# Kernel tuning notes

Measured on AMD Instinct MI355X. Metric: run time of the kernel, lower is better.

## Reference

```python
import jax, jax.numpy as jnp
import numpy as np

N = 50000        # total nodes (disjoint batch of graphs)
E = 800000       # total edges
F_IN = 8         # node feature dim
S = 6            # edge feature dim
H = 20           # ECC kernel-network hidden size (hidden_states)
N_OUT = 20       # ECC output channels (n_out=hidden_states)
G = 32           # GCN channels
D1 = 16          # first dense
N_GRAPHS = 512   # graphs in batch


def setup_inputs() -> dict:
    key = jax.random.key(0)
    ks = jax.random.split(key, 24)
    r = lambda k, sh, s: jax.random.normal(k, sh, dtype=jnp.float32) * s
    return {
        "x": r(ks[0], (N, F_IN), 1.0),
        "e": r(ks[1], (E, S), 1.0),
        "edge_index": jax.random.randint(ks[2], (2, E), 0, N, dtype=jnp.int32),
        "seg": jnp.sort(jax.random.randint(ks[3], (N,), 0, N_GRAPHS, dtype=jnp.int32)),
        # ECC kernel network: S -> H -> H -> F_IN*N_OUT
        "ecc_w1": r(ks[4], (S, H), 0.4), "ecc_b1": jnp.zeros((H,), jnp.float32),
        "ecc_w2": r(ks[5], (H, H), 0.2), "ecc_b2": jnp.zeros((H,), jnp.float32),
        "ecc_w3": r(ks[6], (H, F_IN * N_OUT), 0.2), "ecc_b3": jnp.zeros((F_IN * N_OUT,), jnp.float32),
        "ecc_root": r(ks[7], (F_IN, N_OUT), 0.3), "ecc_b": jnp.zeros((N_OUT,), jnp.float32),
        "gcn1_w": r(ks[8], (N_OUT, G), 0.2), "gcn1_b": jnp.zeros((G,), jnp.float32),
        "gcn2_w": r(ks[9], (G, G), 0.2), "gcn2_b": jnp.zeros((G,), jnp.float32),
        "d1_w": r(ks[10], (G, D1), 0.2), "d1_b": jnp.zeros((D1,), jnp.float32),
        "d2_w": r(ks[11], (D1, 1), 0.2), "d2_b": jnp.zeros((1,), jnp.float32),
    }


def reference(x, e, edge_index, seg,
              ecc_w1, ecc_b1, ecc_w2, ecc_b2, ecc_w3, ecc_b3, ecc_root, ecc_b,
              gcn1_w, gcn1_b, gcn2_w, gcn2_b, d1_w, d1_b, d2_w, d2_b):
    row, col = edge_index[0], edge_index[1]  # message col -> row

    # --- ECCConv: per-edge MLP produces an [F_IN, N_OUT] filter per edge ---
    h = jax.nn.relu(e @ ecc_w1 + ecc_b1)
    h = jax.nn.relu(h @ ecc_w2 + ecc_b2)
    w_edge = (h @ ecc_w3 + ecc_b3).reshape(E, F_IN, N_OUT)   # [E, F_in, F_out]
    msg = jnp.einsum('ef,efo->eo', x[col], w_edge)            # per-edge message
    agg = jax.ops.segment_sum(msg, row, num_segments=N)
    x1 = jax.nn.relu(agg + x @ ecc_root + ecc_b)              # root + bias + relu

    # --- GCN normalization from the edge list (A + I, symmetric norm) ---
    deg = jax.ops.segment_sum(jnp.ones((E,), x.dtype), row, num_segments=N) + 1.0
    dinv = jax.lax.rsqrt(deg)
    edge_norm = (dinv[row] * dinv[col])[:, None]
    self_norm = (dinv * dinv)[:, None]

    def gcn(hin, W, b):
        hw = hin @ W
        nmsg = jax.ops.segment_sum(edge_norm * hw[col], row, num_segments=N)
        return jax.nn.relu(nmsg + self_norm * hw + b)

    x2 = gcn(x1, gcn1_w, gcn1_b)
    x3 = gcn(x2, gcn2_w, gcn2_b)

    # --- GlobalSumPool over graph ids, then MLP head ---
    pooled = jax.ops.segment_sum(x3, seg, num_segments=N_GRAPHS)  # [n_graphs, G]
    out = (pooled @ d1_w + d1_b) @ d2_w + d2_b                    # [n_graphs, 1]
    return out
```

## Files before the change

kernel.cpp:

```cpp
#include <hip/hip_runtime.h>

#define S_DIM   6
#define H_DIM   20
#define F_INN   8
#define N_OUTC  20
#define G_DIM   32
#define D1_DIM  16
#define NGRAPH  512
#define CAP     32
#define COLCAP  2048

typedef short short8 __attribute__((ext_vector_type(8)));
typedef float floatx4 __attribute__((ext_vector_type(4)));

__device__ __forceinline__ unsigned short f2bf(float f) {
    unsigned u = __float_as_uint(f);
    return (unsigned short)((u + 0x8000u) >> 16);
}
__device__ __forceinline__ float bf2f(unsigned short s) {
    return __uint_as_float(((unsigned)s) << 16);
}

__global__ __launch_bounds__(256) void loc_kernel(
    const int* __restrict__ ei, int E, int* __restrict__ cnt,
    int* __restrict__ loc,
    const float* __restrict__ w3, const float* __restrict__ b3,
    unsigned short* __restrict__ B3f)
{
    int i = blockIdx.x * 256 + threadIdx.x;
    if (i < 6144) {
        int jj   = i & 7;
        int n    = (i >> 3) & 15;
        int quad = (i >> 7) & 3;
        int nt   = (i >> 9) & 1;
        int s    = i >> 10;
        int K = 32 * s + quad * 8 + jj;
        int o = n + 16 * nt;
        float v = 0.0f;
        if (o < N_OUTC) {
            if (K < 160)      v = w3[(K >> 3) * 160 + (K & 7) * N_OUTC + o];
            else if (K < 168) v = b3[(K - 160) * N_OUTC + o];
        }
        B3f[i] = f2bf(v);
    }
    if (i >= E) return;
    loc[i] = atomicAdd(&cnt[ei[i]], 1);
}

__global__ __launch_bounds__(256) void scanA_kernel(
    const int* __restrict__ deg, int N, int* __restrict__ bsum)
{
    int i = blockIdx.x * 256 + threadIdx.x;
    int v = (i < N) ? deg[i] : 0;
#pragma unroll
    for (int d = 1; d < 64; d <<= 1) v += __shfl_down(v, d, 64);
    __shared__ int ws[4];
    int wid = threadIdx.x >> 6;
    if ((threadIdx.x & 63) == 0) ws[wid] = v;
    __syncthreads();
    if (threadIdx.x == 0) bsum[blockIdx.x] = ws[0] + ws[1] + ws[2] + ws[3];
}

__global__ __launch_bounds__(256) void scanC_kernel(
    const int* __restrict__ deg, int N, const int* __restrict__ bsum, int nbl,
    int E, int* __restrict__ rowptr)
{
    __shared__ int ws[4];
    __shared__ int sboff;
    int t = threadIdx.x;
    {
        int v = (t < nbl && t < blockIdx.x) ? bsum[t] : 0;
#pragma unroll
        for (int d = 1; d < 64; d <<= 1) v += __shfl_down(v, d, 64);
        int wid = t >> 6;
        if ((t & 63) == 0) ws[wid] = v;
        __syncthreads();
        if (t == 0) sboff = ws[0] + ws[1] + ws[2] + ws[3];
        __syncthreads();
    }

    int i = blockIdx.x * 256 + t;
    int d0 = (i < N) ? deg[i] : 0;
    int v = d0;
#pragma unroll
    for (int d = 1; d < 64; d <<= 1) {
        int u = __shfl_up(v, d, 64);
        if ((t & 63) >= d) v += u;
    }
    __shared__ int ws2[4];
    int wid = t >> 6;
    if ((t & 63) == 63) ws2[wid] = v;
    __syncthreads();
    int woff = 0;
    for (int w = 0; w < wid; ++w) woff += ws2[w];
    if (i < N) rowptr[i] = sboff + woff + v - d0;
    if (blockIdx.x == 0 && t == 0) rowptr[N] = E;
}

__global__ __launch_bounds__(256) void build_kernel(
    const int* __restrict__ ei, int E, const float* __restrict__ e,
    const int* __restrict__ rowptr, const int* __restrict__ loc,
    int4* __restrict__ e_sorted)
{
    int i = blockIdx.x * 256 + threadIdx.x;
    if (i >= E) return;
    int r = ei[i];
    int c = ei[E + i];
    int p = rowptr[r] + loc[i];

    const float2* ep = (const float2*)&e[(size_t)i * S_DIM];
    float2 e0 = ep[0], e1 = ep[1], e2 = ep[2];

    int4 rec;
    rec.x = c;
    rec.y = (int)f2bf(e0.x) | ((int)f2bf(e0.y) << 16);
    rec.z = (int)f2bf(e1.x) | ((int)f2bf(e1.y) << 16);
    rec.w = (int)f2bf(e2.x) | ((int)f2bf(e2.y) << 16);
    e_sorted[p] = rec;
}

__global__ __launch_bounds__(256) void ecc_mfma_kernel(
    const int4* __restrict__ e_sorted, const float* __restrict__ x,
    const int* __restrict__ rowptr, int N, int E,
    const unsigned short* __restrict__ B3f,
    const float* __restrict__ w1, const float* __restrict__ b1,
    const float* __restrict__ w2, const float* __restrict__ b2,
    const float* __restrict__ root, const float* __restrict__ eb,
    const float* __restrict__ g1w,
    float* __restrict__ agg, int* __restrict__ col_sorted,
    unsigned short* __restrict__ hws1)
{
    __shared__ char smem[20480];
    __shared__ float x1buf[CAP * N_OUTC];
    __shared__ int rbounds[2];
    unsigned short (*h2b)[N_OUTC] = (unsigned short (*)[N_OUTC])smem;
    unsigned short (*xb)[F_INN]   = (unsigned short (*)[F_INN])(smem + 10240);
    float* lmsg = (float*)smem;

    int t = threadIdx.x;
    int j0 = blockIdx.x * 256;
    int jend = min(j0 + 256, E);
    int j = j0 + t;

    if (t < 2) {
        int s = (t == 0) ? j0 : (jend - 1);
        int lo = 0, hi = N - 1;
        while (lo < hi) {
            int m = (lo + hi + 1) >> 1;
            if (rowptr[m] <= s) lo = m; else hi = m - 1;
        }
        rbounds[t] = lo;
    }

    if (j < E) {
        int4 rec = e_sorted[j];
        int c = rec.x;
        col_sorted[j] = c;
        float ef[S_DIM] = {
            bf2f((unsigned short)(rec.y & 0xffff)),
            bf2f((unsigned short)((unsigned)rec.y >> 16)),
            bf2f((unsigned short)(rec.z & 0xffff)),
            bf2f((unsigned short)((unsigned)rec.z >> 16)),
            bf2f((unsigned short)(rec.w & 0xffff)),
            bf2f((unsigned short)((unsigned)rec.w >> 16))
        };

        float h1[H_DIM];
#pragma unroll
        for (int jj = 0; jj < H_DIM; ++jj) {
            float a = b1[jj];
#pragma unroll
            for (int s = 0; s < S_DIM; ++s) a = fmaf(ef[s], w1[s * H_DIM + jj], a);
            h1[jj] = fmaxf(a, 0.0f);
        }

        float h2[H_DIM];
#pragma unroll
        for (int jj = 0; jj < H_DIM; ++jj) {
            float a = b2[jj];
#pragma unroll
            for (int k = 0; k < H_DIM; ++k) a = fmaf(h1[k], w2[k * H_DIM + jj], a);
            h2[jj] = fmaxf(a, 0.0f);
        }

        const float4* xp = (const float4*)&x[(size_t)c * F_INN];
        float4 xa = xp[0], xb4 = xp[1];
        float xf[F_INN] = {xa.x, xa.y, xa.z, xa.w, xb4.x, xb4.y, xb4.z, xb4.w};

#pragma unroll
        for (int o = 0; o < N_OUTC; ++o) h2b[t][o] = f2bf(h2[o]);
#pragma unroll
        for (int f = 0; f < F_INN; ++f) xb[t][f] = f2bf(xf[f]);
    } else {
#pragma unroll
        for (int o = 0; o < N_OUTC; ++o) h2b[t][o] = 0;
#pragma unroll
        for (int f = 0; f < F_INN; ++f) xb[t][f] = 0;
    }
    __syncthreads();

    int lane = t & 63;
    int quad = lane >> 4;
    int n = lane & 15;
    const short8* Bg = (const short8*)B3f;
    short8 Bf[12];
#pragma unroll
    for (int s = 0; s < 6; ++s)
#pragma unroll
        for (int nt = 0; nt < 2; ++nt)
            Bf[s * 2 + nt] = Bg[((s * 2 + nt) * 4 + quad) * 16 + n];

    int w = t >> 6;
    floatx4 acc0s[4], acc1s[4];
#pragma unroll
    for (int T = 0; T < 4; ++T) {
        int base = w * 64 + T * 16;
        int m = base + n;

        const short8 xv8 = *(const short8*)&xb[m][0];
        float xfl[F_INN];
#pragma unroll
        for (int jj = 0; jj < F_INN; ++jj) xfl[jj] = bf2f((unsigned short)xv8[jj]);

        floatx4 acc0 = {0.f, 0.f, 0.f, 0.f};
        floatx4 acc1 = {0.f, 0.f, 0.f, 0.f};
#pragma unroll
        for (int s = 0; s < 6; ++s) {
            short8 A = {0, 0, 0, 0, 0, 0, 0, 0};
            if (s < 5) {
                float h = bf2f(h2b[m][4 * s + quad]);
#pragma unroll
                for (int jj = 0; jj < F_INN; ++jj)
                    A[jj] = (short)f2bf(h * xfl[jj]);
            } else if (quad == 0) {
                A = xv8;
            }
            acc0 = __builtin_amdgcn_mfma_f32_16x16x32_bf16(A, Bf[s * 2 + 0], acc0, 0, 0, 0);
            acc1 = __builtin_amdgcn_mfma_f32_16x16x32_bf16(A, Bf[s * 2 + 1], acc1, 0, 0, 0);
        }
        acc0s[T] = acc0;
        acc1s[T] = acc1;
    }
    __syncthreads();

#pragma unroll
    for (int T = 0; T < 4; ++T) {
        int base = w * 64 + T * 16;
#pragma unroll
        for (int r = 0; r < 4; ++r) {
            int row = base + quad * 4 + r;
            lmsg[row * N_OUTC + n] = acc0s[T][r];
            if (n < 4) lmsg[row * N_OUTC + 16 + n] = acc1s[T][r];
        }
    }
    __syncthreads();

    int r0 = rbounds[0], r1 = rbounds[1];
    int nrows = r1 - r0 + 1;
    int work = nrows * 5;
    for (int ww = t; ww < work; ww += 256) {
        int idx = ww / 5;
        int q = ww - idx * 5;
        int row = r0 + idx;
        int a0 = rowptr[row], a1 = rowptr[row + 1];
        int s0 = max(a0, j0), s1 = min(a1, jend);
        float ac0 = 0.f, ac1 = 0.f, ac2 = 0.f, ac3 = 0.f;
        for (int s = s0; s < s1; ++s) {
            const float4 v = *(const float4*)&lmsg[(s - j0) * N_OUTC + q * 4];
            ac0 += v.x; ac1 += v.y; ac2 += v.z; ac3 += v.w;
        }
        bool owned = (a0 >= j0 && a1 <= jend);
        if (owned && idx < CAP) {
            const float4* xp = (const float4*)&x[(size_t)row * F_INN];
            float4 xa = xp[0], xb4 = xp[1];
            float rx[F_INN] = {xa.x, xa.y, xa.z, xa.w, xb4.x, xb4.y, xb4.z, xb4.w};
            float av[4] = {ac0, ac1, ac2, ac3};
#pragma unroll
            for (int u = 0; u < 4; ++u) {
                int oc = q * 4 + u;
                float a = av[u] + eb[oc];
#pragma unroll
                for (int f = 0; f < F_INN; ++f)
                    a = fmaf(rx[f], root[f * N_OUTC + oc], a);
                x1buf[idx * N_OUTC + oc] = fmaxf(a, 0.0f);
            }
        } else {
            float* dst = &agg[(size_t)row * N_OUTC + q * 4];
            if (owned) {
                *(float4*)dst = make_float4(ac0, ac1, ac2, ac3);
            } else {
                unsafeAtomicAdd(dst + 0, ac0);
                unsafeAtomicAdd(dst + 1, ac1);
                unsafeAtomicAdd(dst + 2, ac2);
                unsafeAtomicAdd(dst + 3, ac3);
            }
        }
    }
    __syncthreads();

    int fast = min(nrows, CAP);
    int work2 = fast * 8;
    for (int ww = t; ww < work2; ww += 256) {
        int idx = ww >> 3;
        int qc = ww & 7;
        int row = r0 + idx;
        int a0 = rowptr[row], a1 = rowptr[row + 1];
        if (!(a0 >= j0 && a1 <= jend)) continue;
        float di = rsqrtf((float)(a1 - a0) + 1.0f);
        float m0 = 0.f, m1 = 0.f, m2 = 0.f, m3 = 0.f;
        const float* xr = &x1buf[idx * N_OUTC];
#pragma unroll
        for (int o = 0; o < N_OUTC; ++o) {
            float xv = xr[o];
            const float4 g = *(const float4*)&g1w[o * G_DIM + qc * 4];
            m0 = fmaf(xv, g.x, m0); m1 = fmaf(xv, g.y, m1);
            m2 = fmaf(xv, g.z, m2); m3 = fmaf(xv, g.w, m3);
        }
        unsigned lo32 = (unsigned)f2bf(m0 * di) | ((unsigned)f2bf(m1 * di) << 16);
        unsigned hi32 = (unsigned)f2bf(m2 * di) | ((unsigned)f2bf(m3 * di) << 16);
        *(uint2*)&hws1[(size_t)row * G_DIM + qc * 4] = make_uint2(lo32, hi32);
    }
}

__global__ __launch_bounds__(256) void cleanup_kernel(
    const float* __restrict__ agg, const float* __restrict__ x,
    const int* __restrict__ rowptr, int N,
    const float* __restrict__ root, const float* __restrict__ eb,
    const float* __restrict__ g1w,
    unsigned short* __restrict__ hws1)
{
    int n = blockIdx.x * 256 + threadIdx.x;
    if (n >= N) return;
    int a0 = rowptr[n], a1 = rowptr[n + 1];
    bool contained = (a1 > a0) ? ((a0 >> 8) == ((a1 - 1) >> 8))
                               : ((a0 & 255) != 0);
    if (contained) {
        int target = (a0 >> 8) << 8;
        int lo = 0, hi = N - 1;
        while (lo < hi) {
            int m = (lo + hi + 1) >> 1;
            if (rowptr[m] <= target) lo = m; else hi = m - 1;
        }
        if (n - lo < CAP) return;
    }

    const float4* xp = (const float4*)&x[(size_t)n * F_INN];
    float4 xa = xp[0], xb = xp[1];
    float xf[F_INN] = {xa.x, xa.y, xa.z, xa.w, xb.x, xb.y, xb.z, xb.w};

    float x1[N_OUTC];
#pragma unroll
    for (int o = 0; o < N_OUTC; ++o) {
        float a = agg[(size_t)n * N_OUTC + o] + eb[o];
#pragma unroll
        for (int f = 0; f < F_INN; ++f) a = fmaf(xf[f], root[f * N_OUTC + o], a);
        x1[o] = fmaxf(a, 0.0f);
    }

    float di = rsqrtf((float)(a1 - a0) + 1.0f);
#pragma unroll
    for (int q = 0; q < 4; ++q) {
        short8 o8;
#pragma unroll
        for (int u = 0; u < 8; ++u) {
            int g = q * 8 + u;
            float a = 0.0f;
#pragma unroll
            for (int o = 0; o < N_OUTC; ++o) a = fmaf(x1[o], g1w[o * G_DIM + g], a);
            o8[u] = (short)f2bf(a * di);
        }
        *(short8*)&hws1[(size_t)n * G_DIM + q * 8] = o8;
    }
}

template<bool DO_MATMUL, bool DO_POOL>
__global__ __launch_bounds__(256) void gcn_gather_kernel(
    const unsigned short* __restrict__ hws, const int* __restrict__ rowptr,
    const int* __restrict__ col_sorted, const int* __restrict__ seg, int N,
    const float* __restrict__ bias, const float* __restrict__ w2,
    unsigned short* __restrict__ outbuf, float* __restrict__ pooled)
{
    __shared__ int colbuf[COLCAP];
    __shared__ int binfo[2];
    __shared__ float x2s[DO_MATMUL ? 64 * 33 : 1];
    __shared__ float w2s[DO_MATMUL ? G_DIM * G_DIM : 1];
    __shared__ float pbuf[DO_POOL ? 64 * G_DIM : 1];
    __shared__ int ginfo[2];

    int t = threadIdx.x;
    int n0 = blockIdx.x * 64;
    int nend = min(n0 + 64, N);

    if (t == 0) { binfo[0] = rowptr[n0]; binfo[1] = rowptr[nend]; }
    if (DO_MATMUL) ((float4*)w2s)[t] = ((const float4*)w2)[t];
    if (DO_POOL) {
        if (t == 0) {
            int gmin = seg[n0];
            int gmax = seg[nend - 1];
            ginfo[0] = gmin;
            ginfo[1] = (gmax - gmin < 64) ? 1 : 0;
        }
        for (int k = t; k < 64 * G_DIM; k += 256) pbuf[k] = 0.0f;
    }
    __syncthreads();

    int jb0 = binfo[0];
    int cap = min(binfo[1] - jb0, COLCAP);
    for (int k = t; k < cap; k += 256) colbuf[k] = col_sorted[jb0 + k];
    __syncthreads();

    int nl = t >> 2;
    int q = t & 3;
    int n = n0 + nl;

    float xo[8];
    float di = 0.0f;
    if (n < N) {
        int j0 = rowptr[n], j1 = rowptr[n + 1];
        di = rsqrtf((float)(j1 - j0) + 1.0f);
        short8 sv = *(const short8*)&hws[(size_t)n * G_DIM + q * 8];
        float s[8];
#pragma unroll
        for (int k = 0; k < 8; ++k) s[k] = bf2f((unsigned short)sv[k]);
#pragma unroll 2
        for (int j = j0; j < j1; ++j) {
            int idx = j - jb0;
            int c = (idx < COLCAP) ? colbuf[idx] : col_sorted[j];
            short8 v = *(const short8*)&hws[(size_t)c * G_DIM + q * 8];
#pragma unroll
            for (int k = 0; k < 8; ++k) s[k] += bf2f((unsigned short)v[k]);
        }
#pragma unroll
        for (int k = 0; k < 8; ++k)
            xo[k] = fmaxf(fmaf(di, s[k], bias[q * 8 + k]), 0.0f);
    } else {
#pragma unroll
        for (int k = 0; k < 8; ++k) xo[k] = 0.0f;
    }

    if (DO_MATMUL) {
#pragma unroll
        for (int k = 0; k < 8; ++k) x2s[nl * 33 + q * 8 + k] = xo[k];
        __syncthreads();
        if (n < N) {
            float a[8];
#pragma unroll
            for (int k = 0; k < 8; ++k) a[k] = 0.0f;
#pragma unroll
            for (int g = 0; g < G_DIM; ++g) {
                float xv = x2s[nl * 33 + g];
#pragma unroll
                for (int k = 0; k < 8; ++k)
                    a[k] = fmaf(xv, w2s[g * G_DIM + q * 8 + k], a[k]);
            }
            short8 o8;
#pragma unroll
            for (int k = 0; k < 8; ++k) o8[k] = (short)f2bf(a[k] * di);
            *(short8*)&outbuf[(size_t)n * G_DIM + q * 8] = o8;
        }
    } else if (DO_POOL) {
        int gmin = ginfo[0];
        int use_lds = ginfo[1];
        if (n < N) {
            int sg = seg[n];
            if (use_lds) {
                float* base = &pbuf[(sg - gmin) * G_DIM + q * 8];
#pragma unroll
                for (int k = 0; k < 8; ++k) atomicAdd(&base[k], xo[k]);
            } else {
#pragma unroll
                for (int k = 0; k < 8; ++k)
                    unsafeAtomicAdd(&pooled[(size_t)sg * G_DIM + q * 8 + k], xo[k]);
            }
        }
        __syncthreads();
        if (use_lds) {
            for (int k = t; k < 64 * G_DIM; k += 256) {
                float v = pbuf[k];
                int g = gmin + (k >> 5);
                if (v != 0.0f && g < NGRAPH)
                    unsafeAtomicAdd(&pooled[(size_t)g * G_DIM + (k & 31)], v);
            }
        }
    } else {
        if (n < N) {
            short8 o8;
#pragma unroll
            for (int k = 0; k < 8; ++k) o8[k] = (short)f2bf(xo[k]);
            *(short8*)&outbuf[(size_t)n * G_DIM + q * 8] = o8;
        }
    }
}

__global__ __launch_bounds__(256) void head_kernel(
    const float* __restrict__ pooled,
    const float* __restrict__ d1w, const float* __restrict__ d1b,
    const float* __restrict__ d2w, const float* __restrict__ d2b,
    float* __restrict__ out)
{
    int i = blockIdx.x * 256 + threadIdx.x;
    if (i >= NGRAPH) return;

    float p[G_DIM];
#pragma unroll
    for (int g = 0; g < G_DIM; ++g) p[g] = pooled[i * G_DIM + g];

    float acc = d2b[0];
#pragma unroll
    for (int j = 0; j < D1_DIM; ++j) {
        float tj = d1b[j];
#pragma unroll
        for (int g = 0; g < G_DIM; ++g) tj = fmaf(p[g], d1w[g * D1_DIM + j], tj);
        acc = fmaf(tj, d2w[j], acc);
    }
    out[i] = acc;
}

extern "C" void kernel_launch(void* const* d_in, const int* in_sizes, int n_in,
                              void* d_out, int out_size, void* d_ws, size_t ws_size,
                              hipStream_t stream)
{
    const float* x    = (const float*)d_in[0];
    const float* e    = (const float*)d_in[1];
    const int*   ei   = (const int*)d_in[2];
    const int*   seg  = (const int*)d_in[3];
    const float* w1   = (const float*)d_in[4];
    const float* b1   = (const float*)d_in[5];
    const float* w2   = (const float*)d_in[6];
    const float* b2   = (const float*)d_in[7];
    const float* w3   = (const float*)d_in[8];
    const float* b3   = (const float*)d_in[9];
    const float* root = (const float*)d_in[10];
    const float* eb   = (const float*)d_in[11];
    const float* g1w  = (const float*)d_in[12];
    const float* g1b  = (const float*)d_in[13];
    const float* g2w  = (const float*)d_in[14];
    const float* g2b  = (const float*)d_in[15];
    const float* d1w  = (const float*)d_in[16];
    const float* d1b  = (const float*)d_in[17];
    const float* d2w  = (const float*)d_in[18];
    const float* d2b  = (const float*)d_in[19];

    const int N = in_sizes[3];
    const int E = in_sizes[1] / S_DIM;
    float* out = (float*)d_out;

    const int nbl = (N + 255) / 256;
    const int ebl = (E + 255) / 256;

    char* ws = (char*)d_ws;
    size_t off = 0;
    auto alloc = [&](size_t elems) -> char* {
        char* p = ws + off;
        off += ((elems * 4 + 15) & ~(size_t)15);
        return p;
    };
    int*   cnt        = (int*)  alloc(N);
    float* agg        = (float*)alloc((size_t)N * N_OUTC);
    float* pooled     = (float*)alloc(NGRAPH * G_DIM);
    size_t zero_bytes = off;
    int*   rowptr     = (int*)  alloc(N + 1);
    int*   bsum       = (int*)  alloc(nbl);
    int*   loc        = (int*)  alloc(E);
    int*   col_sorted = (int*)  alloc(E);
    unsigned short* B3f = (unsigned short*)alloc(6144 / 2);
    int4*  e_sorted   = (int4*) alloc((size_t)E * 4);
    unsigned short* hws1 = (unsigned short*)alloc((size_t)N * G_DIM / 2);
    unsigned short* hws2 = (unsigned short*)alloc((size_t)N * G_DIM / 2);
    (void)ws_size;

    hipMemsetAsync(d_ws, 0, zero_bytes, stream);

    loc_kernel<<<ebl, 256, 0, stream>>>(ei, E, cnt, loc, w3, b3, B3f);
    scanA_kernel<<<nbl, 256, 0, stream>>>(cnt, N, bsum);
    scanC_kernel<<<nbl, 256, 0, stream>>>(cnt, N, bsum, nbl, E, rowptr);
    build_kernel<<<ebl, 256, 0, stream>>>(ei, E, e, rowptr, loc, e_sorted);
    ecc_mfma_kernel<<<ebl, 256, 0, stream>>>(e_sorted, x, rowptr, N, E, B3f,
                                             w1, b1, w2, b2, root, eb, g1w,
                                             agg, col_sorted, hws1);
    cleanup_kernel<<<nbl, 256, 0, stream>>>(agg, x, rowptr, N, root, eb, g1w, hws1);
    gcn_gather_kernel<true, false><<<(N + 63) / 64, 256, 0, stream>>>(
        hws1, rowptr, col_sorted, seg, N, g1b, g2w, hws2, nullptr);
    gcn_gather_kernel<false, true><<<(N + 63) / 64, 256, 0, stream>>>(
        hws2, rowptr, col_sorted, seg, N, g2b, nullptr, nullptr, pooled);
    head_kernel<<<(NGRAPH + 255) / 256, 256, 0, stream>>>(pooled, d1w, d1b, d2w, d2b, out);
}
```

Before: 267.1 us.

## Use cursor atomics for CSR build, packed bf16 converts, unrolled GCN gather

The per-edge loc array is dropped. The histogram kernel now only counts, and the build kernel claims CSR slots with an atomic cursor initialised during the scan, which saves one E-sized write and read. All float-to-bf16 conversions switch to the packed round-to-nearest intrinsic. The GCN gather drops its LDS column staging and reads col_sorted directly, unrolled by four to expose more independent loads. The cursor atomics make the order of edges within a row nondeterministic, and the extra atomic traffic in the build kernel could cost about as much as it saves.

```diff
diff --git a/kernel.cpp b/kernel.cpp
--- a/kernel.cpp
+++ b/kernel.cpp
@@ -1,4 +1,5 @@
 #include <hip/hip_runtime.h>
+#include <hip/hip_bf16.h>
 
 #define S_DIM   6
 #define H_DIM   20
@@ -8,7 +9,6 @@
 #define D1_DIM  16
 #define NGRAPH  512
 #define CAP     32
-#define COLCAP  2048
 
 typedef short short8 __attribute__((ext_vector_type(8)));
 typedef float floatx4 __attribute__((ext_vector_type(4)));
@@ -20,10 +20,14 @@
 __device__ __forceinline__ float bf2f(unsigned short s) {
     return __uint_as_float(((unsigned)s) << 16);
 }
-
-__global__ __launch_bounds__(256) void loc_kernel(
+__device__ __forceinline__ unsigned pk2bf(float a, float b) {
+    union { __hip_bfloat162 b2; unsigned u; } cv;
+    cv.b2 = __float22bfloat162_rn(make_float2(a, b));
+    return cv.u;
+}
+
+__global__ __launch_bounds__(256) void hist_kernel(
     const int* __restrict__ ei, int E, int* __restrict__ cnt,
-    int* __restrict__ loc,
     const float* __restrict__ w3, const float* __restrict__ b3,
     unsigned short* __restrict__ B3f)
 {
@@ -44,7 +48,7 @@
         B3f[i] = f2bf(v);
     }
     if (i >= E) return;
-    loc[i] = atomicAdd(&cnt[ei[i]], 1);
+    atomicAdd(&cnt[ei[i]], 1);
 }
 
 __global__ __launch_bounds__(256) void scanA_kernel(
@@ -63,7 +67,7 @@
 
 __global__ __launch_bounds__(256) void scanC_kernel(
     const int* __restrict__ deg, int N, const int* __restrict__ bsum, int nbl,
-    int E, int* __restrict__ rowptr)
+    int E, int* __restrict__ rowptr, int* __restrict__ cursor)
 {
     __shared__ int ws[4];
     __shared__ int sboff;
@@ -93,29 +97,32 @@
     __syncthreads();
     int woff = 0;
     for (int w = 0; w < wid; ++w) woff += ws2[w];
-    if (i < N) rowptr[i] = sboff + woff + v - d0;
+    if (i < N) {
+        int rp = sboff + woff + v - d0;
+        rowptr[i] = rp;
+        cursor[i] = rp;
+    }
     if (blockIdx.x == 0 && t == 0) rowptr[N] = E;
 }
 
 __global__ __launch_bounds__(256) void build_kernel(
     const int* __restrict__ ei, int E, const float* __restrict__ e,
-    const int* __restrict__ rowptr, const int* __restrict__ loc,
-    int4* __restrict__ e_sorted)
+    int* __restrict__ cursor, int4* __restrict__ e_sorted)
 {
     int i = blockIdx.x * 256 + threadIdx.x;
     if (i >= E) return;
     int r = ei[i];
     int c = ei[E + i];
-    int p = rowptr[r] + loc[i];
+    int p = atomicAdd(&cursor[r], 1);
 
     const float2* ep = (const float2*)&e[(size_t)i * S_DIM];
     float2 e0 = ep[0], e1 = ep[1], e2 = ep[2];
 
     int4 rec;
     rec.x = c;
-    rec.y = (int)f2bf(e0.x) | ((int)f2bf(e0.y) << 16);
-    rec.z = (int)f2bf(e1.x) | ((int)f2bf(e1.y) << 16);
-    rec.w = (int)f2bf(e2.x) | ((int)f2bf(e2.y) << 16);
+    rec.y = (int)pk2bf(e0.x, e0.y);
+    rec.z = (int)pk2bf(e1.x, e1.y);
+    rec.w = (int)pk2bf(e2.x, e2.y);
     e_sorted[p] = rec;
 }
 
@@ -188,14 +195,16 @@
         float xf[F_INN] = {xa.x, xa.y, xa.z, xa.w, xb4.x, xb4.y, xb4.z, xb4.w};
 
 #pragma unroll
-        for (int o = 0; o < N_OUTC; ++o) h2b[t][o] = f2bf(h2[o]);
-#pragma unroll
-        for (int f = 0; f < F_INN; ++f) xb[t][f] = f2bf(xf[f]);
+        for (int p = 0; p < N_OUTC / 2; ++p)
+            *(unsigned*)&h2b[t][2 * p] = pk2bf(h2[2 * p], h2[2 * p + 1]);
+#pragma unroll
+        for (int p = 0; p < F_INN / 2; ++p)
+            *(unsigned*)&xb[t][2 * p] = pk2bf(xf[2 * p], xf[2 * p + 1]);
     } else {
 #pragma unroll
-        for (int o = 0; o < N_OUTC; ++o) h2b[t][o] = 0;
-#pragma unroll
-        for (int f = 0; f < F_INN; ++f) xb[t][f] = 0;
+        for (int p = 0; p < N_OUTC / 2; ++p) *(unsigned*)&h2b[t][2 * p] = 0u;
+#pragma unroll
+        for (int p = 0; p < F_INN / 2; ++p)  *(unsigned*)&xb[t][2 * p] = 0u;
     }
     __syncthreads();
 
@@ -229,9 +238,11 @@
             short8 A = {0, 0, 0, 0, 0, 0, 0, 0};
             if (s < 5) {
                 float h = bf2f(h2b[m][4 * s + quad]);
-#pragma unroll
-                for (int jj = 0; jj < F_INN; ++jj)
-                    A[jj] = (short)f2bf(h * xfl[jj]);
+                union { short8 s8; unsigned u[4]; } av;
+#pragma unroll
+                for (int p = 0; p < 4; ++p)
+                    av.u[p] = pk2bf(h * xfl[2 * p], h * xfl[2 * p + 1]);
+                A = av.s8;
             } else if (quad == 0) {
                 A = xv8;
             }
@@ -316,8 +327,8 @@
             m0 = fmaf(xv, g.x, m0); m1 = fmaf(xv, g.y, m1);
             m2 = fmaf(xv, g.z, m2); m3 = fmaf(xv, g.w, m3);
         }
-        unsigned lo32 = (unsigned)f2bf(m0 * di) | ((unsigned)f2bf(m1 * di) << 16);
-        unsigned hi32 = (unsigned)f2bf(m2 * di) | ((unsigned)f2bf(m3 * di) << 16);
+        unsigned lo32 = pk2bf(m0 * di, m1 * di);
+        unsigned hi32 = pk2bf(m2 * di, m3 * di);
         *(uint2*)&hws1[(size_t)row * G_DIM + qc * 4] = make_uint2(lo32, hi32);
     }
 }
@@ -360,16 +371,19 @@
     float di = rsqrtf((float)(a1 - a0) + 1.0f);
 #pragma unroll
     for (int q = 0; q < 4; ++q) {
-        short8 o8;
+        float a[8];
 #pragma unroll
         for (int u = 0; u < 8; ++u) {
             int g = q * 8 + u;
-            float a = 0.0f;
-#pragma unroll
-            for (int o = 0; o < N_OUTC; ++o) a = fmaf(x1[o], g1w[o * G_DIM + g], a);
-            o8[u] = (short)f2bf(a * di);
-        }
-        *(short8*)&hws1[(size_t)n * G_DIM + q * 8] = o8;
+            float acc = 0.0f;
+#pragma unroll
+            for (int o = 0; o < N_OUTC; ++o) acc = fmaf(x1[o], g1w[o * G_DIM + g], acc);
+            a[u] = acc * di;
+        }
+        union { short8 s8; unsigned u4[4]; } ov;
+#pragma unroll
+        for (int p = 0; p < 4; ++p) ov.u4[p] = pk2bf(a[2 * p], a[2 * p + 1]);
+        *(short8*)&hws1[(size_t)n * G_DIM + q * 8] = ov.s8;
     }
 }
 
@@ -380,8 +394,6 @@
     const float* __restrict__ bias, const float* __restrict__ w2,
     unsigned short* __restrict__ outbuf, float* __restrict__ pooled)
 {
-    __shared__ int colbuf[COLCAP];
-    __shared__ int binfo[2];
     __shared__ float x2s[DO_MATMUL ? 64 * 33 : 1];
     __shared__ float w2s[DO_MATMUL ? G_DIM * G_DIM : 1];
     __shared__ float pbuf[DO_POOL ? 64 * G_DIM : 1];
@@ -391,7 +403,6 @@
     int n0 = blockIdx.x * 64;
     int nend = min(n0 + 64, N);
 
-    if (t == 0) { binfo[0] = rowptr[n0]; binfo[1] = rowptr[nend]; }
     if (DO_MATMUL) ((float4*)w2s)[t] = ((const float4*)w2)[t];
     if (DO_POOL) {
         if (t == 0) {
@@ -402,12 +413,7 @@
         }
         for (int k = t; k < 64 * G_DIM; k += 256) pbuf[k] = 0.0f;
     }
-    __syncthreads();
-
-    int jb0 = binfo[0];
-    int cap = min(binfo[1] - jb0, COLCAP);
-    for (int k = t; k < cap; k += 256) colbuf[k] = col_sorted[jb0 + k];
-    __syncthreads();
+    if (DO_MATMUL || DO_POOL) __syncthreads();
 
     int nl = t >> 2;
     int q = t & 3;
@@ -422,10 +428,23 @@
         float s[8];
 #pragma unroll
         for (int k = 0; k < 8; ++k) s[k] = bf2f((unsigned short)sv[k]);
-#pragma unroll 2
-        for (int j = j0; j < j1; ++j) {
-            int idx = j - jb0;
-            int c = (idx < COLCAP) ? colbuf[idx] : col_sorted[j];
+        int j = j0;
+        for (; j + 4 <= j1; j += 4) {
+            int c0 = col_sorted[j + 0];
+            int c1 = col_sorted[j + 1];
+            int c2 = col_sorted[j + 2];
+            int c3 = col_sorted[j + 3];
+            short8 v0 = *(const short8*)&hws[(size_t)c0 * G_DIM + q * 8];
+            short8 v1 = *(const short8*)&hws[(size_t)c1 * G_DIM + q * 8];
+            short8 v2 = *(const short8*)&hws[(size_t)c2 * G_DIM + q * 8];
+            short8 v3 = *(const short8*)&hws[(size_t)c3 * G_DIM + q * 8];
+#pragma unroll
+            for (int k = 0; k < 8; ++k)
+                s[k] += (bf2f((unsigned short)v0[k]) + bf2f((unsigned short)v1[k]))
+                      + (bf2f((unsigned short)v2[k]) + bf2f((unsigned short)v3[k]));
+        }
+        for (; j < j1; ++j) {
+            int c = col_sorted[j];
             short8 v = *(const short8*)&hws[(size_t)c * G_DIM + q * 8];
 #pragma unroll
             for (int k = 0; k < 8; ++k) s[k] += bf2f((unsigned short)v[k]);
@@ -453,10 +472,10 @@
                 for (int k = 0; k < 8; ++k)
                     a[k] = fmaf(xv, w2s[g * G_DIM + q * 8 + k], a[k]);
             }
-            short8 o8;
-#pragma unroll
-            for (int k = 0; k < 8; ++k) o8[k] = (short)f2bf(a[k] * di);
-            *(short8*)&outbuf[(size_t)n * G_DIM + q * 8] = o8;
+            union { short8 s8; unsigned u4[4]; } ov;
+#pragma unroll
+            for (int p = 0; p < 4; ++p) ov.u4[p] = pk2bf(a[2 * p] * di, a[2 * p + 1] * di);
+            *(short8*)&outbuf[(size_t)n * G_DIM + q * 8] = ov.s8;
         }
     } else if (DO_POOL) {
         int gmin = ginfo[0];
@@ -484,10 +503,10 @@
         }
     } else {
         if (n < N) {
-            short8 o8;
-#pragma unroll
-            for (int k = 0; k < 8; ++k) o8[k] = (short)f2bf(xo[k]);
-            *(short8*)&outbuf[(size_t)n * G_DIM + q * 8] = o8;
+            union { short8 s8; unsigned u4[4]; } ov;
+#pragma unroll
+            for (int p = 0; p < 4; ++p) ov.u4[p] = pk2bf(xo[2 * p], xo[2 * p + 1]);
+            *(short8*)&outbuf[(size_t)n * G_DIM + q * 8] = ov.s8;
         }
     }
 }
@@ -560,8 +579,8 @@
     float* pooled     = (float*)alloc(NGRAPH * G_DIM);
     size_t zero_bytes = off;
     int*   rowptr     = (int*)  alloc(N + 1);
+    int*   cursor     = (int*)  alloc(N);
     int*   bsum       = (int*)  alloc(nbl);
-    int*   loc        = (int*)  alloc(E);
     int*   col_sorted = (int*)  alloc(E);
     unsigned short* B3f = (unsigned short*)alloc(6144 / 2);
     int4*  e_sorted   = (int4*) alloc((size_t)E * 4);
@@ -571,10 +590,10 @@
 
     hipMemsetAsync(d_ws, 0, zero_bytes, stream);
 
-    loc_kernel<<<ebl, 256, 0, stream>>>(ei, E, cnt, loc, w3, b3, B3f);
+    hist_kernel<<<ebl, 256, 0, stream>>>(ei, E, cnt, w3, b3, B3f);
     scanA_kernel<<<nbl, 256, 0, stream>>>(cnt, N, bsum);
-    scanC_kernel<<<nbl, 256, 0, stream>>>(cnt, N, bsum, nbl, E, rowptr);
-    build_kernel<<<ebl, 256, 0, stream>>>(ei, E, e, rowptr, loc, e_sorted);
+    scanC_kernel<<<nbl, 256, 0, stream>>>(cnt, N, bsum, nbl, E, rowptr, cursor);
+    build_kernel<<<ebl, 256, 0, stream>>>(ei, E, e, cursor, e_sorted);
     ecc_mfma_kernel<<<ebl, 256, 0, stream>>>(e_sorted, x, rowptr, N, E, B3f,
                                              w1, b1, w2, b2, root, eb, g1w,
                                              agg, col_sorted, hws1);
```

Result: slower. 297.7 us (+11.4%).
